# Optimization experiments

Measured on AMD Instinct MI355X. Metric: run time of the kernel, lower is better.

The kernel has to match this reference:

```python
import jax, jax.numpy as jnp
import numpy as np

EMBED_DIM = 768
NUM_HEADS = 12
HEAD_DIM = EMBED_DIM // NUM_HEADS
SCALING = HEAD_DIM ** -0.5
LN_EPS = 1e-5
B, T, S = 2, 2048, 2048


def setup_inputs() -> dict:
    key = jax.random.key(0)
    ks = jax.random.split(key, 16)
    d = EMBED_DIM
    std = 1.0 / np.sqrt(d)
    inp = {
        "query": jax.random.normal(ks[0], (B, T, d), jnp.float32),
        "key": jax.random.normal(ks[1], (B, S, d), jnp.float32),
        "value": jax.random.normal(ks[2], (B, S, d), jnp.float32),
        "key_padding_mask": jax.random.randint(ks[3], (B, S), 0, 2, jnp.int32),
        "attn_mask": jnp.zeros((T, S), jnp.float32),
        "relative_pos": jax.random.normal(ks[4], (B, NUM_HEADS, T, S), jnp.float32),
        # projection params (linear_1 branch of each Beit3Linear; split_position=-1)
        "Wq": jax.random.normal(ks[5], (d, d), jnp.float32) * std,
        "bq": jnp.zeros((d,), jnp.float32),
        "Wk": jax.random.normal(ks[6], (d, d), jnp.float32) * std,
        "bk": jnp.zeros((d,), jnp.float32),
        "Wv": jax.random.normal(ks[7], (d, d), jnp.float32) * std,
        "bv": jnp.zeros((d,), jnp.float32),
        "Wo": jax.random.normal(ks[8], (d, d), jnp.float32) * std,
        "bo": jnp.zeros((d,), jnp.float32),
        # inner_attn_ln (subln=True), layernorm_1 branch
        "ln_g": jnp.ones((d,), jnp.float32),
        "ln_b": jnp.zeros((d,), jnp.float32),
    }
    return inp


def _layernorm(x, g, b):
    mu = jnp.mean(x, axis=-1, keepdims=True)
    var = jnp.var(x, axis=-1, keepdims=True)
    return (x - mu) * jax.lax.rsqrt(var + LN_EPS) * g + b


def reference(query, key, value, key_padding_mask, attn_mask, relative_pos,
              Wq, bq, Wk, bk, Wv, bv, Wo, bo, ln_g, ln_b):
    b, t, d = query.shape
    s = key.shape[1]
    h, hd = NUM_HEADS, HEAD_DIM

    q = ((query @ Wq.T + bq) * SCALING).reshape(b, t, h, hd).transpose(0, 2, 1, 3)  # [b,h,t,hd]
    k = (key @ Wk.T + bk).reshape(b, s, h, hd).transpose(0, 2, 1, 3)                # [b,h,s,hd]
    v = (value @ Wv.T + bv).reshape(b, s, h, hd).transpose(0, 2, 1, 3)              # [b,h,s,hd]

    scores = jnp.einsum("bhtd,bhsd->bhts", q, k)
    # attn_mask path: nan_to_num then additive broadcast over batch*heads
    scores = jnp.nan_to_num(scores) + attn_mask[None, None, :, :]
    # key padding mask: True -> -inf over all heads/queries
    kpm = key_padding_mask.astype(bool)[:, None, None, :]
    scores = jnp.where(kpm, -jnp.inf, scores)
    # relative position bias
    scores = scores + relative_pos

    # float32 softmax, cast back
    attn_weights = jax.nn.softmax(scores.astype(jnp.float32), axis=-1).astype(scores.dtype)

    attn = jnp.einsum("bhts,bhsd->bhtd", attn_weights, v)  # dropout p=0
    attn = attn.transpose(0, 2, 1, 3).reshape(b, t, d)
    attn = _layernorm(attn, ln_g, ln_b)
    attn = attn @ Wo.T + bo

    attn_weights_out = attn_weights.transpose(1, 0, 2, 3)  # [h,b,t,s]
    return attn, attn_weights_out
```

## Files before the change

### kernel.cpp

```cpp
#include <hip/hip_runtime.h>
#include <hip/hip_bf16.h>

typedef __attribute__((ext_vector_type(8))) __bf16 bf16x8;
typedef __attribute__((ext_vector_type(4))) __bf16 bf16x4;
typedef __attribute__((ext_vector_type(4))) float f32x4;

#define MFMA16(a, b, c) __builtin_amdgcn_mfma_f32_16x16x32_bf16((a), (b), (c), 0, 0, 0)

__global__ __launch_bounds__(256) void cast_kernel(
    const float* __restrict__ xq, const float* __restrict__ xk,
    const float* __restrict__ xv, const float* __restrict__ Wq,
    const float* __restrict__ Wk, const float* __restrict__ Wv,
    const float* __restrict__ Wo, __bf16* __restrict__ oxq,
    __bf16* __restrict__ oxk, __bf16* __restrict__ oxv,
    __bf16* __restrict__ owq, __bf16* __restrict__ owk,
    __bf16* __restrict__ owv, __bf16* __restrict__ owo) {
  int bid = blockIdx.x;
  const float* src;
  __bf16* dst;
  int base;
  if (bid < 3072) { src = xq; dst = oxq; base = bid; }
  else if (bid < 6144) { src = xk; dst = oxk; base = bid - 3072; }
  else if (bid < 9216) { src = xv; dst = oxv; base = bid - 6144; }
  else if (bid < 9792) { src = Wq; dst = owq; base = bid - 9216; }
  else if (bid < 10368) { src = Wk; dst = owk; base = bid - 9792; }
  else if (bid < 10944) { src = Wv; dst = owv; base = bid - 10368; }
  else { src = Wo; dst = owo; base = bid - 10944; }
  int idx = base * 256 + threadIdx.x;
  float4 v = *(const float4*)&src[idx * 4];
  bf16x4 o;
  o[0] = (__bf16)v.x; o[1] = (__bf16)v.y; o[2] = (__bf16)v.z; o[3] = (__bf16)v.w;
  *(bf16x4*)&dst[idx * 4] = o;
}

__global__ __launch_bounds__(64) void qkv_kernel(
    const __bf16* __restrict__ xq, const __bf16* __restrict__ xk,
    const __bf16* __restrict__ xv, const __bf16* __restrict__ wq,
    const __bf16* __restrict__ wk, const __bf16* __restrict__ wvp,
    const float* __restrict__ bq, const float* __restrict__ bk,
    const float* __restrict__ bv, __bf16* __restrict__ qo,
    __bf16* __restrict__ ko, __bf16* __restrict__ vo) {
  int wg = blockIdx.x;
  int p = wg / 768;
  int wgi = wg - p * 768;
  const __bf16* X = (p == 0) ? xq : (p == 1) ? xk : xv;
  const __bf16* W = (p == 0) ? wq : (p == 1) ? wk : wvp;
  const float* bias = (p == 0) ? bq : (p == 1) ? bk : bv;
  __bf16* out = (p == 0) ? qo : (p == 1) ? ko : vo;
  float scale = (p == 0) ? 0.125f : 1.0f;
  int vmode = (p == 2);

  int lane = threadIdx.x & 63;
  int lr = lane & 15, kg = lane >> 4;
  int mt = wgi / 12, nt = wgi - mt * 12;
  int m0 = mt * 64, n0 = nt * 64;
  f32x4 acc[4][4];
#pragma unroll
  for (int i = 0; i < 4; i++)
#pragma unroll
    for (int j = 0; j < 4; j++) acc[i][j] = (f32x4){0.f, 0.f, 0.f, 0.f};

  for (int k0 = 0; k0 < 768; k0 += 32) {
    bf16x8 af[4], bw[4];
#pragma unroll
    for (int i = 0; i < 4; i++) {
      af[i] = *(const bf16x8*)(X + (size_t)(m0 + i * 16 + lr) * 768 + k0 + kg * 8);
      bw[i] = *(const bf16x8*)(W + (size_t)(n0 + i * 16 + lr) * 768 + k0 + kg * 8);
    }
#pragma unroll
    for (int i = 0; i < 4; i++)
#pragma unroll
      for (int j = 0; j < 4; j++) acc[i][j] = MFMA16(af[i], bw[j], acc[i][j]);
  }

  int h = nt;
#pragma unroll
  for (int i = 0; i < 4; i++)
#pragma unroll
    for (int j = 0; j < 4; j++)
#pragma unroll
      for (int r = 0; r < 4; r++) {
        int m = m0 + i * 16 + kg * 4 + r;
        int hd = j * 16 + lr;
        float v = (acc[i][j][r] + bias[n0 + hd]) * scale;
        int b = m >> 11, pos = m & 2047;
        size_t idx;
        if (!vmode)
          idx = ((size_t)(b * 12 + h) * 2048 + pos) * 64 + hd;
        else
          idx = ((size_t)(b * 12 + h) * 64 + hd) * 2048 + pos;
        out[idx] = (__bf16)v;
      }
}

__global__ __launch_bounds__(1024, 8) void attn_kernel(
    const __bf16* __restrict__ qw, const __bf16* __restrict__ kw,
    const __bf16* __restrict__ vT, const int* __restrict__ kpm,
    const float* __restrict__ amask, const float* __restrict__ rpos,
    float* __restrict__ wout, float* __restrict__ attn_pre) {
  __shared__ __align__(16) unsigned char smem[16 * 2056 * 2];
  __shared__ __align__(16) float bias[2048];
  __shared__ float invA[16];
  auto sc = (__bf16(*)[2056])smem;
  auto pl = (float(*)[4][16][16])smem;

  int wg = blockIdx.x;
  int qt = wg & 127, bh = wg >> 7;
  int b = bh / 12, h = bh - b * 12;
  int t0 = qt * 16;
  int wv = threadIdx.x >> 6, lane = threadIdx.x & 63;
  int lr = lane & 15, kg = lane >> 4;

  const __bf16* qp = qw + (size_t)bh * 2048 * 64;
  const __bf16* kp = kw + (size_t)bh * 2048 * 64;
  const __bf16* vp = vT + (size_t)bh * 64 * 2048;

  int m = wv;
  int t = t0 + m;
  const float* rp = rpos + ((size_t)bh * 2048 + t) * 2048;

  {
    int i0 = threadIdx.x * 2;
    int2 kk = *(const int2*)&kpm[b * 2048 + i0];
    bias[i0] = kk.x ? -__builtin_inff() : 0.0f;
    bias[i0 + 1] = kk.y ? -__builtin_inff() : 0.0f;
  }

  float4 rb[4];
#pragma unroll
  for (int i = 0; i < 4; i++) rb[i] = *(const float4*)&rp[lane * 4 + 256 * i];

  bf16x8 a0 = *(const bf16x8*)(qp + (size_t)(t0 + lr) * 64 + kg * 8);
  bf16x8 a1 = *(const bf16x8*)(qp + (size_t)(t0 + lr) * 64 + 32 + kg * 8);
  for (int nt = wv; nt < 128; nt += 16) {
    int s0 = nt * 16;
    bf16x8 b0 = *(const bf16x8*)(kp + (size_t)(s0 + lr) * 64 + kg * 8);
    bf16x8 b1 = *(const bf16x8*)(kp + (size_t)(s0 + lr) * 64 + 32 + kg * 8);
    f32x4 c = (f32x4){0.f, 0.f, 0.f, 0.f};
    c = MFMA16(a0, b0, c);
    c = MFMA16(a1, b1, c);
#pragma unroll
    for (int r = 0; r < 4; r++) sc[kg * 4 + r][s0 + lr] = (__bf16)c[r];
  }
  __syncthreads();

  const float* am = amask + (size_t)t * 2048;
  float sum = 0.f;
  bf16x4 ereg[8];
  {
#pragma unroll
    for (int i = 0; i < 8; i++) {
      int c = lane * 4 + 256 * i;
      float4 r4 = rb[i & 3];
      if (i < 4) rb[i] = *(const float4*)&rp[c + 1024];
      float4 a4 = *(const float4*)&am[c];
      bf16x4 sv = *(const bf16x4*)&sc[m][c];
      float4 b4 = *(const float4*)&bias[c];
      float4 e4;
      e4.x = __expf((float)sv[0] + a4.x + r4.x + b4.x);
      e4.y = __expf((float)sv[1] + a4.y + r4.y + b4.y);
      e4.z = __expf((float)sv[2] + a4.z + r4.z + b4.z);
      e4.w = __expf((float)sv[3] + a4.w + r4.w + b4.w);
      bf16x4 ev;
      ev[0] = (__bf16)e4.x; ev[1] = (__bf16)e4.y;
      ev[2] = (__bf16)e4.z; ev[3] = (__bf16)e4.w;
      ereg[i] = ev;
      *(bf16x4*)&sc[m][c] = ev;
      sum += e4.x + e4.y + e4.z + e4.w;
    }
#pragma unroll
    for (int o = 32; o >= 1; o >>= 1) sum += __shfl_xor(sum, o);
    if (lane == 0) invA[m] = 1.0f / sum;
  }
  __syncthreads();

  {
    float inv = 1.0f / sum;
    float* wr = wout + ((size_t)(h * 2 + b) * 2048 + t) * 2048;
#pragma unroll
    for (int i = 0; i < 8; i++) {
      int c = lane * 4 + 256 * i;
      bf16x4 ev = ereg[i];
      float4 w4;
      w4.x = (float)ev[0] * inv; w4.y = (float)ev[1] * inv;
      w4.z = (float)ev[2] * inv; w4.w = (float)ev[3] * inv;
      *(float4*)&wr[c] = w4;
    }
  }

  f32x4 acc = (f32x4){0.f, 0.f, 0.f, 0.f};
  {
    int jt = wv & 3, kc = wv >> 2;
    for (int ks = kc * 16; ks < kc * 16 + 16; ks++) {
      bf16x8 af = *(const bf16x8*)&sc[lr][ks * 32 + kg * 8];
      bf16x8 bv = *(const bf16x8*)(vp + (size_t)(jt * 16 + lr) * 2048 + ks * 32 + kg * 8);
      acc = MFMA16(af, bv, acc);
    }
  }
  __syncthreads();
  {
    int jt = wv & 3, kc = wv >> 2;
#pragma unroll
    for (int r = 0; r < 4; r++) pl[kc][jt][kg * 4 + r][lr] = acc[r];
  }
  __syncthreads();
  {
    int row = threadIdx.x >> 6;
    int cc = threadIdx.x & 63;
    int jj = cc >> 4, col = cc & 15;
    float s = (pl[0][jj][row][col] + pl[1][jj][row][col] +
               pl[2][jj][row][col] + pl[3][jj][row][col]) * invA[row];
    attn_pre[((size_t)b * 2048 + t0 + row) * 768 + h * 64 + cc] = s;
  }
}

__global__ __launch_bounds__(256) void ln_kernel(
    const float* __restrict__ x, const float* __restrict__ g,
    const float* __restrict__ be, __bf16* __restrict__ out) {
  int row = blockIdx.x * 4 + (threadIdx.x >> 6);
  int lane = threadIdx.x & 63;
  const float* xr = x + (size_t)row * 768;
  float v[12];
  float s = 0.f;
#pragma unroll
  for (int i = 0; i < 12; i++) {
    v[i] = xr[lane + 64 * i];
    s += v[i];
  }
#pragma unroll
  for (int o = 32; o >= 1; o >>= 1) s += __shfl_xor(s, o);
  float mu = s * (1.0f / 768.0f);
  float var = 0.f;
#pragma unroll
  for (int i = 0; i < 12; i++) {
    float d = v[i] - mu;
    var += d * d;
  }
#pragma unroll
  for (int o = 32; o >= 1; o >>= 1) var += __shfl_xor(var, o);
  var *= (1.0f / 768.0f);
  float rs = rsqrtf(var + 1e-5f);
#pragma unroll
  for (int i = 0; i < 12; i++) {
    int c = lane + 64 * i;
    out[(size_t)row * 768 + c] = (__bf16)((v[i] - mu) * rs * g[c] + be[c]);
  }
}

__global__ __launch_bounds__(256) void oproj_kernel(
    const __bf16* __restrict__ Xb, const __bf16* __restrict__ W,
    const float* __restrict__ bias, float* __restrict__ out) {
  __shared__ float pl[4][64][65];
  int wv = threadIdx.x >> 6;
  int lane = threadIdx.x & 63;
  int lr = lane & 15, kg = lane >> 4;
  int tile = blockIdx.x;
  int mt = tile / 12, nt = tile - mt * 12;
  int m0 = mt * 64, n0 = nt * 64;
  f32x4 acc[4][4];
#pragma unroll
  for (int i = 0; i < 4; i++)
#pragma unroll
    for (int j = 0; j < 4; j++) acc[i][j] = (f32x4){0.f, 0.f, 0.f, 0.f};

  int k0b = wv * 192;
  for (int k0 = k0b; k0 < k0b + 192; k0 += 32) {
    bf16x8 af[4], bw[4];
#pragma unroll
    for (int i = 0; i < 4; i++) {
      af[i] = *(const bf16x8*)(Xb + (size_t)(m0 + i * 16 + lr) * 768 + k0 + kg * 8);
      bw[i] = *(const bf16x8*)(W + (size_t)(n0 + i * 16 + lr) * 768 + k0 + kg * 8);
    }
#pragma unroll
    for (int i = 0; i < 4; i++)
#pragma unroll
      for (int j = 0; j < 4; j++) acc[i][j] = MFMA16(af[i], bw[j], acc[i][j]);
  }

#pragma unroll
  for (int i = 0; i < 4; i++)
#pragma unroll
    for (int j = 0; j < 4; j++)
#pragma unroll
      for (int r = 0; r < 4; r++)
        pl[wv][i * 16 + kg * 4 + r][j * 16 + lr] = acc[i][j][r];
  __syncthreads();
#pragma unroll
  for (int e = 0; e < 16; e++) {
    int idx = threadIdx.x + e * 256;
    int mm = idx >> 6, nn = idx & 63;
    float s = pl[0][mm][nn] + pl[1][mm][nn] + pl[2][mm][nn] + pl[3][mm][nn];
    out[(size_t)(m0 + mm) * 768 + n0 + nn] = s + bias[n0 + nn];
  }
}

extern "C" void kernel_launch(void* const* d_in, const int* in_sizes, int n_in,
                              void* d_out, int out_size, void* d_ws, size_t ws_size,
                              hipStream_t stream) {
  const float* query = (const float*)d_in[0];
  const float* key = (const float*)d_in[1];
  const float* value = (const float*)d_in[2];
  const int* kpm = (const int*)d_in[3];
  const float* amask = (const float*)d_in[4];
  const float* rpos = (const float*)d_in[5];
  const float* Wq = (const float*)d_in[6];
  const float* bq = (const float*)d_in[7];
  const float* Wk = (const float*)d_in[8];
  const float* bk = (const float*)d_in[9];
  const float* Wv = (const float*)d_in[10];
  const float* bv = (const float*)d_in[11];
  const float* Wo = (const float*)d_in[12];
  const float* bo = (const float*)d_in[13];
  const float* lng = (const float*)d_in[14];
  const float* lnb = (const float*)d_in[15];

  char* ws = (char*)d_ws;
  __bf16* qw = (__bf16*)ws;
  __bf16* kw = (__bf16*)(ws + 6291456);
  __bf16* vT = (__bf16*)(ws + 12582912);
  float* attn_pre = (float*)(ws + 18874368);
  __bf16* lnx = (__bf16*)(ws + 31457280);
  __bf16* xqb = (__bf16*)(ws + 37748736);
  __bf16* xkb = (__bf16*)(ws + 44040192);
  __bf16* xvb = (__bf16*)(ws + 50331648);
  __bf16* wqb = (__bf16*)(ws + 56623104);
  __bf16* wkb = (__bf16*)(ws + 57802752);
  __bf16* wvb = (__bf16*)(ws + 58982400);
  __bf16* wob = (__bf16*)(ws + 60162048);

  float* out_attn = (float*)d_out;
  float* out_w = out_attn + 3145728;

  cast_kernel<<<11520, dim3(256), 0, stream>>>(query, key, value, Wq, Wk, Wv,
                                               Wo, xqb, xkb, xvb, wqb, wkb,
                                               wvb, wob);
  qkv_kernel<<<2304, dim3(64), 0, stream>>>(xqb, xkb, xvb, wqb, wkb, wvb,
                                            bq, bk, bv, qw, kw, vT);
  attn_kernel<<<3072, dim3(1024), 0, stream>>>(qw, kw, vT, kpm, amask, rpos,
                                               out_w, attn_pre);
  ln_kernel<<<1024, dim3(256), 0, stream>>>(attn_pre, lng, lnb, lnx);
  oproj_kernel<<<768, dim3(256), 0, stream>>>(lnx, wob, bo, out_attn);
}
```

Baseline: 402.1 us.

## Stream relative_pos and attn_mask via async global-to-LDS double buffering

Replaces register prefetch of relative_pos and direct attn_mask loads with asynchronous global_load_lds transfers into double-buffered LDS stages. Explicit vmcnt waits let each 256-column chunk overlap the next chunk's loads. The key padding mask is now applied while scores are written, which removes the shared bias array. The launch-bounds occupancy hint is dropped. The hand-placed waitcnt ordering is fragile and adds LDS traffic.

```diff
diff --git a/kernel.cpp b/kernel.cpp
--- a/kernel.cpp
+++ b/kernel.cpp
@@ -6,6 +6,12 @@
 typedef __attribute__((ext_vector_type(4))) float f32x4;
 
 #define MFMA16(a, b, c) __builtin_amdgcn_mfma_f32_16x16x32_bf16((a), (b), (c), 0, 0, 0)
+
+__device__ __forceinline__ void gl_lds16(const float* g, float* l) {
+  __builtin_amdgcn_global_load_lds(
+      (const __attribute__((address_space(1))) void*)g,
+      (__attribute__((address_space(3))) void*)l, 16, 0, 0);
+}
 
 __global__ __launch_bounds__(256) void cast_kernel(
     const float* __restrict__ xq, const float* __restrict__ xk,
@@ -93,13 +99,14 @@
       }
 }
 
-__global__ __launch_bounds__(1024, 8) void attn_kernel(
+__global__ __launch_bounds__(1024) void attn_kernel(
     const __bf16* __restrict__ qw, const __bf16* __restrict__ kw,
     const __bf16* __restrict__ vT, const int* __restrict__ kpm,
     const float* __restrict__ amask, const float* __restrict__ rpos,
     float* __restrict__ wout, float* __restrict__ attn_pre) {
   __shared__ __align__(16) unsigned char smem[16 * 2056 * 2];
-  __shared__ __align__(16) float bias[2048];
+  __shared__ __align__(16) float rstage[2][16][256];
+  __shared__ __align__(16) float astage[2][16][256];
   __shared__ float invA[16];
   auto sc = (__bf16(*)[2056])smem;
   auto pl = (float(*)[4][16][16])smem;
@@ -118,60 +125,63 @@
   int m = wv;
   int t = t0 + m;
   const float* rp = rpos + ((size_t)bh * 2048 + t) * 2048;
-
-  {
-    int i0 = threadIdx.x * 2;
-    int2 kk = *(const int2*)&kpm[b * 2048 + i0];
-    bias[i0] = kk.x ? -__builtin_inff() : 0.0f;
-    bias[i0 + 1] = kk.y ? -__builtin_inff() : 0.0f;
-  }
-
-  float4 rb[4];
-#pragma unroll
-  for (int i = 0; i < 4; i++) rb[i] = *(const float4*)&rp[lane * 4 + 256 * i];
+  const float* am = amask + (size_t)t * 2048;
+
+  gl_lds16(rp + lane * 4, &rstage[0][wv][0]);
+  gl_lds16(am + lane * 4, &astage[0][wv][0]);
+  gl_lds16(rp + 256 + lane * 4, &rstage[1][wv][0]);
+  gl_lds16(am + 256 + lane * 4, &astage[1][wv][0]);
 
   bf16x8 a0 = *(const bf16x8*)(qp + (size_t)(t0 + lr) * 64 + kg * 8);
   bf16x8 a1 = *(const bf16x8*)(qp + (size_t)(t0 + lr) * 64 + 32 + kg * 8);
+  const float NEGINF = -__builtin_inff();
   for (int nt = wv; nt < 128; nt += 16) {
     int s0 = nt * 16;
     bf16x8 b0 = *(const bf16x8*)(kp + (size_t)(s0 + lr) * 64 + kg * 8);
     bf16x8 b1 = *(const bf16x8*)(kp + (size_t)(s0 + lr) * 64 + 32 + kg * 8);
+    int kk = kpm[(size_t)b * 2048 + s0 + lr];
     f32x4 c = (f32x4){0.f, 0.f, 0.f, 0.f};
     c = MFMA16(a0, b0, c);
     c = MFMA16(a1, b1, c);
 #pragma unroll
-    for (int r = 0; r < 4; r++) sc[kg * 4 + r][s0 + lr] = (__bf16)c[r];
-  }
-  __syncthreads();
-
-  const float* am = amask + (size_t)t * 2048;
+    for (int r = 0; r < 4; r++)
+      sc[kg * 4 + r][s0 + lr] = (__bf16)(kk ? NEGINF : c[r]);
+  }
+  __syncthreads();
+
   float sum = 0.f;
   bf16x4 ereg[8];
-  {
-#pragma unroll
-    for (int i = 0; i < 8; i++) {
-      int c = lane * 4 + 256 * i;
-      float4 r4 = rb[i & 3];
-      if (i < 4) rb[i] = *(const float4*)&rp[c + 1024];
-      float4 a4 = *(const float4*)&am[c];
-      bf16x4 sv = *(const bf16x4*)&sc[m][c];
-      float4 b4 = *(const float4*)&bias[c];
-      float4 e4;
-      e4.x = __expf((float)sv[0] + a4.x + r4.x + b4.x);
-      e4.y = __expf((float)sv[1] + a4.y + r4.y + b4.y);
-      e4.z = __expf((float)sv[2] + a4.z + r4.z + b4.z);
-      e4.w = __expf((float)sv[3] + a4.w + r4.w + b4.w);
-      bf16x4 ev;
-      ev[0] = (__bf16)e4.x; ev[1] = (__bf16)e4.y;
-      ev[2] = (__bf16)e4.z; ev[3] = (__bf16)e4.w;
-      ereg[i] = ev;
-      *(bf16x4*)&sc[m][c] = ev;
-      sum += e4.x + e4.y + e4.z + e4.w;
-    }
-#pragma unroll
-    for (int o = 32; o >= 1; o >>= 1) sum += __shfl_xor(sum, o);
-    if (lane == 0) invA[m] = 1.0f / sum;
-  }
+#define BSTEP(C, WN)                                                          \
+  {                                                                           \
+    asm volatile("s_waitcnt vmcnt(" #WN ")" ::: "memory");                    \
+    __builtin_amdgcn_sched_barrier(0);                                        \
+    float4 r4 = *(const float4*)&rstage[(C) & 1][wv][lane * 4];               \
+    float4 a4 = *(const float4*)&astage[(C) & 1][wv][lane * 4];               \
+    bf16x4 sv = *(const bf16x4*)&sc[wv][(C) * 256 + lane * 4];                \
+    float4 e4;                                                                \
+    e4.x = __expf((float)sv[0] + a4.x + r4.x);                                \
+    e4.y = __expf((float)sv[1] + a4.y + r4.y);                                \
+    e4.z = __expf((float)sv[2] + a4.z + r4.z);                                \
+    e4.w = __expf((float)sv[3] + a4.w + r4.w);                                \
+    asm volatile("s_waitcnt lgkmcnt(0)" ::: "memory");                        \
+    __builtin_amdgcn_sched_barrier(0);                                        \
+    if ((C) < 6) {                                                            \
+      gl_lds16(rp + ((C) + 2) * 256 + lane * 4, &rstage[(C) & 1][wv][0]);     \
+      gl_lds16(am + ((C) + 2) * 256 + lane * 4, &astage[(C) & 1][wv][0]);     \
+    }                                                                         \
+    bf16x4 ev;                                                                \
+    ev[0] = (__bf16)e4.x; ev[1] = (__bf16)e4.y;                               \
+    ev[2] = (__bf16)e4.z; ev[3] = (__bf16)e4.w;                               \
+    ereg[C] = ev;                                                             \
+    *(bf16x4*)&sc[wv][(C) * 256 + lane * 4] = ev;                             \
+    sum += e4.x + e4.y + e4.z + e4.w;                                         \
+  }
+  BSTEP(0, 2); BSTEP(1, 2); BSTEP(2, 2); BSTEP(3, 2);
+  BSTEP(4, 2); BSTEP(5, 2); BSTEP(6, 2); BSTEP(7, 0);
+#undef BSTEP
+#pragma unroll
+  for (int o = 32; o >= 1; o >>= 1) sum += __shfl_xor(sum, o);
+  if (lane == 0) invA[m] = 1.0f / sum;
   __syncthreads();
 
   {
```

New measurement: 438.4 us. +9.0%, slower.
